# Optimization experiments

Measured on AMD Instinct MI355X. Metric: run time of the kernel, lower is better.

## Reference

```python
import jax, jax.numpy as jnp
import numpy as np

N_NODES = 100000
N_EDGES = 625000
D_IN = 128
D_OUT = 128


def setup_inputs() -> dict:
    key = jax.random.key(0)
    k1, k2, k3, k4, k5 = jax.random.split(key, 5)
    feature = jax.random.normal(k1, (N_NODES, D_IN), dtype=jnp.float32)
    W = jax.random.normal(k2, (D_OUT, D_IN), dtype=jnp.float32) * (1.0 / np.sqrt(D_IN))
    b = jax.random.normal(k3, (D_OUT,), dtype=jnp.float32) * 0.01
    src = jax.random.randint(k4, (N_EDGES,), 0, N_NODES, dtype=jnp.int64)
    dst = jax.random.randint(k5, (N_EDGES,), 0, N_NODES, dtype=jnp.int64)
    return {"feature": feature, "W": W, "b": b, "src": src, "dst": dst}


def reference(feature, W, b, src, dst):
    # copy_src: gather source-node features along edges -> [E, D_IN]
    msg = feature[src]
    # mean reduce over incoming edges per destination node
    agg = jax.ops.segment_sum(msg, dst, num_segments=N_NODES)  # [N, D_IN]
    deg = jax.ops.segment_sum(jnp.ones((dst.shape[0],), feature.dtype), dst,
                              num_segments=N_NODES)  # [N]
    # DGL mean leaves nodes with zero in-degree at 0
    h = jnp.where(deg[:, None] > 0, agg / jnp.maximum(deg, 1.0)[:, None], 0.0)
    # nn.Linear: h @ W.T + b
    return h @ W.T + b
```

## Files before the change

### kernel.cpp

```cpp
#include <hip/hip_runtime.h>

#define D 128
#define CAP 32

__device__ __forceinline__ unsigned short f2bf_rne(float x) {
    unsigned int u = __float_as_uint(x);
    u += 0x7fffu + ((u >> 16) & 1u);
    return (unsigned short)(u >> 16);
}

__global__ __launch_bounds__(256)
void pack_bf16(const float* __restrict__ feat, ushort* __restrict__ fb, int n4) {
    int i = blockIdx.x * 256 + threadIdx.x;
    if (i >= n4) return;
    float4 v = ((const float4*)feat)[i];
    ushort4 o;
    o.x = f2bf_rne(v.x); o.y = f2bf_rne(v.y);
    o.z = f2bf_rne(v.z); o.w = f2bf_rne(v.w);
    ((ushort4*)fb)[i] = o;
}

__global__ __launch_bounds__(256)
void transpose_W(const float* __restrict__ W, float* __restrict__ Wt) {
    int tid = blockIdx.x * 256 + threadIdx.x;
    int o = tid >> 7;
    int i = tid & 127;
    Wt[i * D + o] = W[tid];
}

__global__ __launch_bounds__(256)
void build_buckets(const int* __restrict__ src,
                   const int* __restrict__ dst,
                   int* __restrict__ cnt,
                   int* __restrict__ bucket,
                   int n_edges) {
    int e = blockIdx.x * 256 + threadIdx.x;
    if (e >= n_edges) return;
    int d = dst[e];
    int p = atomicAdd(cnt + d, 1);
    if (p < CAP) bucket[(size_t)d * CAP + p] = src[e];
}

__global__ __launch_bounds__(256)
void agg_gemm(const ushort* __restrict__ fb,
              const int* __restrict__ cnt,
              const int* __restrict__ bucket,
              const float* __restrict__ Wt,
              const float* __restrict__ b,
              float* __restrict__ out,
              int n_nodes) {
    __shared__ float hs[32 * D];
    int t = threadIdx.x;
    int lane = t & 63;
    int wave = t >> 6;
    int nb = blockIdx.x * 32;
    int base = nb + wave * 8;

    int myc = 0;
    {
        int nl = base + lane;
        if (lane < 8 && nl < n_nodes) myc = cnt[nl];
    }

    size_t off = (size_t)(lane << 1);

    for (int g = 0; g < 2; ++g) {
        int n0g = base + g * 4;
        int nA = n0g + (lane >> 5);
        int nB = n0g + 2 + (lane >> 5);
        int idsA = (nA < n_nodes) ? bucket[(size_t)nA * CAP + (lane & 31)] : 0;
        int idsB = (nB < n_nodes) ? bucket[(size_t)nB * CAP + (lane & 31)] : 0;
        int d0 = __shfl(myc, g * 4 + 0);
        int d1 = __shfl(myc, g * 4 + 1);
        int d2 = __shfl(myc, g * 4 + 2);
        int d3 = __shfl(myc, g * 4 + 3);
        int m0 = d0 < CAP ? d0 : CAP;
        int m1 = d1 < CAP ? d1 : CAP;
        int m2 = d2 < CAP ? d2 : CAP;
        int m3 = d3 < CAP ? d3 : CAP;
        int mm01 = m0 > m1 ? m0 : m1;
        int mm23 = m2 > m3 ? m2 : m3;
        int mmax = mm01 > mm23 ? mm01 : mm23;

        float ax0 = 0, ay0 = 0, ax1 = 0, ay1 = 0;
        float ax2 = 0, ay2 = 0, ax3 = 0, ay3 = 0;

        for (int j = 0; j < mmax; j += 8) {
            unsigned int v0[8], v1[8], v2[8], v3[8];
#pragma unroll
            for (int i = 0; i < 8; ++i) { v0[i] = 0; v1[i] = 0; v2[i] = 0; v3[i] = 0; }
#pragma unroll
            for (int i = 0; i < 8; ++i)
                if (j + i < m0) { int s = __shfl(idsA, j + i);      v0[i] = *(const unsigned int*)(fb + (size_t)s * D + off); }
#pragma unroll
            for (int i = 0; i < 8; ++i)
                if (j + i < m1) { int s = __shfl(idsA, 32 + j + i); v1[i] = *(const unsigned int*)(fb + (size_t)s * D + off); }
#pragma unroll
            for (int i = 0; i < 8; ++i)
                if (j + i < m2) { int s = __shfl(idsB, j + i);      v2[i] = *(const unsigned int*)(fb + (size_t)s * D + off); }
#pragma unroll
            for (int i = 0; i < 8; ++i)
                if (j + i < m3) { int s = __shfl(idsB, 32 + j + i); v3[i] = *(const unsigned int*)(fb + (size_t)s * D + off); }
#pragma unroll
            for (int i = 0; i < 8; ++i) {
                ax0 += __uint_as_float(v0[i] << 16); ay0 += __uint_as_float(v0[i] & 0xffff0000u);
                ax1 += __uint_as_float(v1[i] << 16); ay1 += __uint_as_float(v1[i] & 0xffff0000u);
                ax2 += __uint_as_float(v2[i] << 16); ay2 += __uint_as_float(v2[i] & 0xffff0000u);
                ax3 += __uint_as_float(v3[i] << 16); ay3 += __uint_as_float(v3[i] & 0xffff0000u);
            }
        }

        float i0 = d0 > 0 ? 1.0f / (float)d0 : 0.0f;
        float i1 = d1 > 0 ? 1.0f / (float)d1 : 0.0f;
        float i2 = d2 > 0 ? 1.0f / (float)d2 : 0.0f;
        float i3 = d3 > 0 ? 1.0f / (float)d3 : 0.0f;
        ((float2*)&hs[(wave * 8 + g * 4 + 0) * D])[lane] = make_float2(ax0 * i0, ay0 * i0);
        ((float2*)&hs[(wave * 8 + g * 4 + 1) * D])[lane] = make_float2(ax1 * i1, ay1 * i1);
        ((float2*)&hs[(wave * 8 + g * 4 + 2) * D])[lane] = make_float2(ax2 * i2, ay2 * i2);
        ((float2*)&hs[(wave * 8 + g * 4 + 3) * D])[lane] = make_float2(ax3 * i3, ay3 * i3);
    }
    __syncthreads();

    int tr = t >> 5;
    int tc = t & 31;
    int n0 = tr * 4;
    int o0 = tc * 4;

    float acc[4][4] = {};
    const float4* Wt4 = (const float4*)Wt;

    for (int c = 0; c < 16; ++c) {
        float hreg[4][8];
#pragma unroll
        for (int m = 0; m < 4; ++m) {
            const float4* hp = (const float4*)&hs[(n0 + m) * D + c * 8];
            float4 a = hp[0], q = hp[1];
            hreg[m][0] = a.x; hreg[m][1] = a.y; hreg[m][2] = a.z; hreg[m][3] = a.w;
            hreg[m][4] = q.x; hreg[m][5] = q.y; hreg[m][6] = q.z; hreg[m][7] = q.w;
        }
#pragma unroll
        for (int j = 0; j < 8; ++j) {
            float4 wv = Wt4[(c * 8 + j) * 32 + tc];
#pragma unroll
            for (int m = 0; m < 4; ++m) {
                acc[m][0] += hreg[m][j] * wv.x;
                acc[m][1] += hreg[m][j] * wv.y;
                acc[m][2] += hreg[m][j] * wv.z;
                acc[m][3] += hreg[m][j] * wv.w;
            }
        }
    }

    float bv0 = b[o0 + 0];
    float bv1 = b[o0 + 1];
    float bv2 = b[o0 + 2];
    float bv3 = b[o0 + 3];
#pragma unroll
    for (int m = 0; m < 4; ++m) {
        int n = nb + n0 + m;
        if (n < n_nodes) {
            float4 o;
            o.x = acc[m][0] + bv0;
            o.y = acc[m][1] + bv1;
            o.z = acc[m][2] + bv2;
            o.w = acc[m][3] + bv3;
            *(float4*)&out[(size_t)n * D + o0] = o;
        }
    }
}

extern "C" void kernel_launch(void* const* d_in, const int* in_sizes, int n_in,
                              void* d_out, int out_size, void* d_ws, size_t ws_size,
                              hipStream_t stream) {
    const float* feat = (const float*)d_in[0];
    const float* W    = (const float*)d_in[1];
    const float* bia  = (const float*)d_in[2];
    const int* src = (const int*)d_in[3];
    const int* dst = (const int*)d_in[4];
    float* out = (float*)d_out;

    int n_nodes = in_sizes[0] / D;
    int n_edges = in_sizes[3];

    size_t cnt_bytes    = (size_t)n_nodes * sizeof(int);
    size_t bucket_bytes = (size_t)n_nodes * CAP * sizeof(int);
    size_t wt_bytes     = (size_t)D * D * sizeof(float);
    int*    cnt    = (int*)d_ws;
    int*    bucket = (int*)((char*)d_ws + cnt_bytes);
    float*  Wt     = (float*)((char*)d_ws + cnt_bytes + bucket_bytes);
    ushort* fb     = (ushort*)((char*)d_ws + cnt_bytes + bucket_bytes + wt_bytes);

    int n4 = n_nodes * (D / 4);

    hipMemsetAsync(cnt, 0, cnt_bytes, stream);
    pack_bf16<<<(n4 + 255) / 256, 256, 0, stream>>>(feat, fb, n4);
    transpose_W<<<(D * D) / 256, 256, 0, stream>>>(W, Wt);
    build_buckets<<<(n_edges + 255) / 256, 256, 0, stream>>>(src, dst, cnt, bucket, n_edges);
    agg_gemm<<<(n_nodes + 31) / 32, 256, 0, stream>>>(fb, cnt, bucket, Wt, bia, out, n_nodes);
}
```

Measured before the change: 216.7 us.

## Use bf16 MFMA for the linear layer and make gather loads unconditional

Replaces the fp32 SIMT matmul with bf16 MFMA 16x16x32 instructions, storing aggregated rows as bf16 in padded shared memory and W as bf16 (no transpose). Merges the W conversion into the feature pack kernel and adds a zero row so out-of-range edge slots gather from it, removing per-load predicates. Drops the node bounds checks, which assumes the node count is a multiple of 32, and rounds the aggregated features to bf16 before the GEMM.

```diff
diff --git a/kernel.cpp b/kernel.cpp
--- a/kernel.cpp
+++ b/kernel.cpp
@@ -2,6 +2,9 @@
 
 #define D 128
 #define CAP 32
+
+typedef __attribute__((ext_vector_type(8))) short short8;
+typedef __attribute__((ext_vector_type(4))) float f32x4;
 
 __device__ __forceinline__ unsigned short f2bf_rne(float x) {
     unsigned int u = __float_as_uint(x);
@@ -10,22 +13,25 @@
 }
 
 __global__ __launch_bounds__(256)
-void pack_bf16(const float* __restrict__ feat, ushort* __restrict__ fb, int n4) {
+void pack_all(const float* __restrict__ feat, const float* __restrict__ W,
+              ushort* __restrict__ fb, ushort* __restrict__ Wb, int n4) {
     int i = blockIdx.x * 256 + threadIdx.x;
-    if (i >= n4) return;
-    float4 v = ((const float4*)feat)[i];
-    ushort4 o;
-    o.x = f2bf_rne(v.x); o.y = f2bf_rne(v.y);
-    o.z = f2bf_rne(v.z); o.w = f2bf_rne(v.w);
-    ((ushort4*)fb)[i] = o;
-}
-
-__global__ __launch_bounds__(256)
-void transpose_W(const float* __restrict__ W, float* __restrict__ Wt) {
-    int tid = blockIdx.x * 256 + threadIdx.x;
-    int o = tid >> 7;
-    int i = tid & 127;
-    Wt[i * D + o] = W[tid];
+    if (i < n4) {
+        float4 v = ((const float4*)feat)[i];
+        ushort4 o;
+        o.x = f2bf_rne(v.x); o.y = f2bf_rne(v.y);
+        o.z = f2bf_rne(v.z); o.w = f2bf_rne(v.w);
+        ((ushort4*)fb)[i] = o;
+    } else if (i < n4 + 32) {
+        ((ushort4*)fb)[i] = make_ushort4(0, 0, 0, 0);
+    } else if (i < n4 + 32 + 4096) {
+        int j = i - (n4 + 32);
+        float4 v = ((const float4*)W)[j];
+        ushort4 o;
+        o.x = f2bf_rne(v.x); o.y = f2bf_rne(v.y);
+        o.z = f2bf_rne(v.z); o.w = f2bf_rne(v.w);
+        ((ushort4*)Wb)[j] = o;
+    }
 }
 
 __global__ __launch_bounds__(256)
@@ -45,31 +51,27 @@
 void agg_gemm(const ushort* __restrict__ fb,
               const int* __restrict__ cnt,
               const int* __restrict__ bucket,
-              const float* __restrict__ Wt,
+              const ushort* __restrict__ Wb,
               const float* __restrict__ b,
               float* __restrict__ out,
               int n_nodes) {
-    __shared__ float hs[32 * D];
+    __shared__ ushort hs[32 * 136];
     int t = threadIdx.x;
     int lane = t & 63;
     int wave = t >> 6;
     int nb = blockIdx.x * 32;
     int base = nb + wave * 8;
 
-    int myc = 0;
-    {
-        int nl = base + lane;
-        if (lane < 8 && nl < n_nodes) myc = cnt[nl];
-    }
+    int myc = (lane < 8) ? cnt[base + lane] : 0;
 
-    size_t off = (size_t)(lane << 1);
+    const ushort* fbl = fb + (size_t)(lane << 1);
 
     for (int g = 0; g < 2; ++g) {
         int n0g = base + g * 4;
         int nA = n0g + (lane >> 5);
         int nB = n0g + 2 + (lane >> 5);
-        int idsA = (nA < n_nodes) ? bucket[(size_t)nA * CAP + (lane & 31)] : 0;
-        int idsB = (nB < n_nodes) ? bucket[(size_t)nB * CAP + (lane & 31)] : 0;
+        int idsA = bucket[(size_t)nA * CAP + (lane & 31)];
+        int idsB = bucket[(size_t)nB * CAP + (lane & 31)];
         int d0 = __shfl(myc, g * 4 + 0);
         int d1 = __shfl(myc, g * 4 + 1);
         int d2 = __shfl(myc, g * 4 + 2);
@@ -78,6 +80,10 @@
         int m1 = d1 < CAP ? d1 : CAP;
         int m2 = d2 < CAP ? d2 : CAP;
         int m3 = d3 < CAP ? d3 : CAP;
+        int mA = (lane < 32) ? m0 : m1;
+        int mB = (lane < 32) ? m2 : m3;
+        idsA = ((lane & 31) < mA) ? idsA : n_nodes;
+        idsB = ((lane & 31) < mB) ? idsB : n_nodes;
         int mm01 = m0 > m1 ? m0 : m1;
         int mm23 = m2 > m3 ? m2 : m3;
         int mmax = mm01 > mm23 ? mm01 : mm23;
@@ -88,19 +94,16 @@
         for (int j = 0; j < mmax; j += 8) {
             unsigned int v0[8], v1[8], v2[8], v3[8];
 #pragma unroll
-            for (int i = 0; i < 8; ++i) { v0[i] = 0; v1[i] = 0; v2[i] = 0; v3[i] = 0; }
-#pragma unroll
-            for (int i = 0; i < 8; ++i)
-                if (j + i < m0) { int s = __shfl(idsA, j + i);      v0[i] = *(const unsigned int*)(fb + (size_t)s * D + off); }
-#pragma unroll
-            for (int i = 0; i < 8; ++i)
-                if (j + i < m1) { int s = __shfl(idsA, 32 + j + i); v1[i] = *(const unsigned int*)(fb + (size_t)s * D + off); }
-#pragma unroll
-            for (int i = 0; i < 8; ++i)
-                if (j + i < m2) { int s = __shfl(idsB, j + i);      v2[i] = *(const unsigned int*)(fb + (size_t)s * D + off); }
-#pragma unroll
-            for (int i = 0; i < 8; ++i)
-                if (j + i < m3) { int s = __shfl(idsB, 32 + j + i); v3[i] = *(const unsigned int*)(fb + (size_t)s * D + off); }
+            for (int i = 0; i < 8; ++i) {
+                int s0 = __shfl(idsA, j + i);
+                int s1 = __shfl(idsA, 32 + j + i);
+                int s2 = __shfl(idsB, j + i);
+                int s3 = __shfl(idsB, 32 + j + i);
+                v0[i] = *(const unsigned int*)(fbl + (size_t)s0 * D);
+                v1[i] = *(const unsigned int*)(fbl + (size_t)s1 * D);
+                v2[i] = *(const unsigned int*)(fbl + (size_t)s2 * D);
+                v3[i] = *(const unsigned int*)(fbl + (size_t)s3 * D);
+            }
 #pragma unroll
             for (int i = 0; i < 8; ++i) {
                 ax0 += __uint_as_float(v0[i] << 16); ay0 += __uint_as_float(v0[i] & 0xffff0000u);
@@ -114,57 +117,39 @@
         float i1 = d1 > 0 ? 1.0f / (float)d1 : 0.0f;
         float i2 = d2 > 0 ? 1.0f / (float)d2 : 0.0f;
         float i3 = d3 > 0 ? 1.0f / (float)d3 : 0.0f;
-        ((float2*)&hs[(wave * 8 + g * 4 + 0) * D])[lane] = make_float2(ax0 * i0, ay0 * i0);
-        ((float2*)&hs[(wave * 8 + g * 4 + 1) * D])[lane] = make_float2(ax1 * i1, ay1 * i1);
-        ((float2*)&hs[(wave * 8 + g * 4 + 2) * D])[lane] = make_float2(ax2 * i2, ay2 * i2);
-        ((float2*)&hs[(wave * 8 + g * 4 + 3) * D])[lane] = make_float2(ax3 * i3, ay3 * i3);
+        unsigned int* hsu = (unsigned int*)hs;
+        int r0 = wave * 8 + g * 4;
+        hsu[(r0 + 0) * 68 + lane] = ((unsigned int)f2bf_rne(ay0 * i0) << 16) | f2bf_rne(ax0 * i0);
+        hsu[(r0 + 1) * 68 + lane] = ((unsigned int)f2bf_rne(ay1 * i1) << 16) | f2bf_rne(ax1 * i1);
+        hsu[(r0 + 2) * 68 + lane] = ((unsigned int)f2bf_rne(ay2 * i2) << 16) | f2bf_rne(ax2 * i2);
+        hsu[(r0 + 3) * 68 + lane] = ((unsigned int)f2bf_rne(ay3 * i3) << 16) | f2bf_rne(ax3 * i3);
     }
     __syncthreads();
 
-    int tr = t >> 5;
-    int tc = t & 31;
-    int n0 = tr * 4;
-    int o0 = tc * 4;
+    int mt = wave & 1;
+    int nh = wave >> 1;
+    int lane16 = lane & 15;
+    int lq = lane >> 4;
 
-    float acc[4][4] = {};
-    const float4* Wt4 = (const float4*)Wt;
-
-    for (int c = 0; c < 16; ++c) {
-        float hreg[4][8];
+    f32x4 acc[4] = {{0,0,0,0},{0,0,0,0},{0,0,0,0},{0,0,0,0}};
 #pragma unroll
-        for (int m = 0; m < 4; ++m) {
-            const float4* hp = (const float4*)&hs[(n0 + m) * D + c * 8];
-            float4 a = hp[0], q = hp[1];
-            hreg[m][0] = a.x; hreg[m][1] = a.y; hreg[m][2] = a.z; hreg[m][3] = a.w;
-            hreg[m][4] = q.x; hreg[m][5] = q.y; hreg[m][6] = q.z; hreg[m][7] = q.w;
-        }
+    for (int ks = 0; ks < 4; ++ks) {
+        short8 afrg = *(const short8*)&hs[(mt * 16 + lane16) * 136 + ks * 32 + lq * 8];
 #pragma unroll
-        for (int j = 0; j < 8; ++j) {
-            float4 wv = Wt4[(c * 8 + j) * 32 + tc];
-#pragma unroll
-            for (int m = 0; m < 4; ++m) {
-                acc[m][0] += hreg[m][j] * wv.x;
-                acc[m][1] += hreg[m][j] * wv.y;
-                acc[m][2] += hreg[m][j] * wv.z;
-                acc[m][3] += hreg[m][j] * wv.w;
-            }
+        for (int tt = 0; tt < 4; ++tt) {
+            short8 bfrg = *(const short8*)&Wb[(size_t)(nh * 64 + tt * 16 + lane16) * D + ks * 32 + lq * 8];
+            acc[tt] = __builtin_amdgcn_mfma_f32_16x16x32_bf16(afrg, bfrg, acc[tt], 0, 0, 0);
         }
     }
 
-    float bv0 = b[o0 + 0];
-    float bv1 = b[o0 + 1];
-    float bv2 = b[o0 + 2];
-    float bv3 = b[o0 + 3];
 #pragma unroll
-    for (int m = 0; m < 4; ++m) {
-        int n = nb + n0 + m;
-        if (n < n_nodes) {
-            float4 o;
-            o.x = acc[m][0] + bv0;
-            o.y = acc[m][1] + bv1;
-            o.z = acc[m][2] + bv2;
-            o.w = acc[m][3] + bv3;
-            *(float4*)&out[(size_t)n * D + o0] = o;
+    for (int tt = 0; tt < 4; ++tt) {
+        int o = nh * 64 + tt * 16 + lane16;
+        float bb = b[o];
+        int node = nb + mt * 16 + lq * 4;
+#pragma unroll
+        for (int r = 0; r < 4; ++r) {
+            out[(size_t)(node + r) * D + o] = acc[tt][r] + bb;
         }
     }
 }
@@ -182,19 +167,23 @@
     int n_nodes = in_sizes[0] / D;
     int n_edges = in_sizes[3];
 
-    size_t cnt_bytes    = (size_t)n_nodes * sizeof(int);
-    size_t bucket_bytes = (size_t)n_nodes * CAP * sizeof(int);
-    size_t wt_bytes     = (size_t)D * D * sizeof(float);
-    int*    cnt    = (int*)d_ws;
-    int*    bucket = (int*)((char*)d_ws + cnt_bytes);
-    float*  Wt     = (float*)((char*)d_ws + cnt_bytes + bucket_bytes);
-    ushort* fb     = (ushort*)((char*)d_ws + cnt_bytes + bucket_bytes + wt_bytes);
+    size_t off = 0;
+    auto alloc = [&](size_t bytes) { size_t p = off; off = (off + bytes + 4095) & ~(size_t)4095; return p; };
+    size_t cnt_off    = alloc((size_t)n_nodes * sizeof(int));
+    size_t bucket_off = alloc((size_t)n_nodes * CAP * sizeof(int));
+    size_t wb_off     = alloc((size_t)D * D * sizeof(ushort));
+    size_t fb_off     = alloc((size_t)(n_nodes + 1) * D * sizeof(ushort));
+
+    int*    cnt    = (int*)((char*)d_ws + cnt_off);
+    int*    bucket = (int*)((char*)d_ws + bucket_off);
+    ushort* Wb     = (ushort*)((char*)d_ws + wb_off);
+    ushort* fb     = (ushort*)((char*)d_ws + fb_off);
 
     int n4 = n_nodes * (D / 4);
+    int G  = n4 + 32 + (D * D / 4);
 
-    hipMemsetAsync(cnt, 0, cnt_bytes, stream);
-    pack_bf16<<<(n4 + 255) / 256, 256, 0, stream>>>(feat, fb, n4);
-    transpose_W<<<(D * D) / 256, 256, 0, stream>>>(W, Wt);
+    hipMemsetAsync(cnt, 0, (size_t)n_nodes * sizeof(int), stream);
+    pack_all<<<(G + 255) / 256, 256, 0, stream>>>(feat, W, fb, Wb, n4);
     build_buckets<<<(n_edges + 255) / 256, 256, 0, stream>>>(src, dst, cnt, bucket, n_edges);
-    agg_gemm<<<(n_nodes + 31) / 32, 256, 0, stream>>>(fb, cnt, bucket, Wt, bia, out, n_nodes);
+    agg_gemm<<<n_nodes / 32, 256, 0, stream>>>(fb, cnt, bucket, Wb, bia, out, n_nodes);
 }
```

Measured after the change: 191.0 us. 1.13x faster.
